# Optimization experiments

Hardware: AMD Instinct MI355X
Metric: run time of the kernel (lower is better)

The kernel has to match this reference:

```python
import jax, jax.numpy as jnp
import numpy as np

HIDDEN = 4096
N_HEADS = 32
N_KV_HEADS = 8
HEAD_DIM = HIDDEN // N_HEADS  # 128
GROUPS = N_HEADS // N_KV_HEADS  # 4
ROPE_BASE = 10000.0
BATCH, SEQ = 1, 2048


def _rope_cos_sin(position_ids, dim, base):
    # position_ids: [b, s] int -> cos/sin [b, s, dim]
    inv_freq = 1.0 / (base ** (jnp.arange(0, dim, 2, dtype=jnp.float32) / dim))  # [dim/2]
    freqs = position_ids.astype(jnp.float32)[..., None] * inv_freq  # [b, s, dim/2]
    emb = jnp.concatenate([freqs, freqs], axis=-1)  # [b, s, dim]
    return jnp.cos(emb), jnp.sin(emb)


def _rotate_half(x):
    x1, x2 = jnp.split(x, 2, axis=-1)
    return jnp.concatenate([-x2, x1], axis=-1)


def setup_inputs() -> dict:
    key = jax.random.key(0)
    ks = jax.random.split(key, 8)
    s = 0.02
    return {
        'hidden_states': jax.random.normal(ks[0], (BATCH, SEQ, HIDDEN), dtype=jnp.float32),
        'position_ids': jnp.broadcast_to(jnp.arange(SEQ, dtype=jnp.int64), (BATCH, SEQ)),
        'Wq': jax.random.normal(ks[1], (HIDDEN, N_HEADS * HEAD_DIM), dtype=jnp.float32) * s,
        'bq': jax.random.normal(ks[2], (N_HEADS * HEAD_DIM,), dtype=jnp.float32) * s,
        'Wk': jax.random.normal(ks[3], (HIDDEN, N_KV_HEADS * HEAD_DIM), dtype=jnp.float32) * s,
        'bk': jax.random.normal(ks[4], (N_KV_HEADS * HEAD_DIM,), dtype=jnp.float32) * s,
        'Wv': jax.random.normal(ks[5], (HIDDEN, N_KV_HEADS * HEAD_DIM), dtype=jnp.float32) * s,
        'bv': jax.random.normal(ks[6], (N_KV_HEADS * HEAD_DIM,), dtype=jnp.float32) * s,
        'Wo': jax.random.normal(ks[7], (HIDDEN, HIDDEN), dtype=jnp.float32) * s,
    }


def reference(hidden_states, position_ids, Wq, bq, Wk, bk, Wv, bv, Wo):
    b, s, _ = hidden_states.shape
    # QKV projections (bias=True for q/k/v per module)
    q = hidden_states @ Wq + bq  # [b, s, H*d]
    k = hidden_states @ Wk + bk  # [b, s, Hk*d]
    v = hidden_states @ Wv + bv  # [b, s, Hk*d]
    q = q.reshape(b, s, N_HEADS, HEAD_DIM)
    k = k.reshape(b, s, N_KV_HEADS, HEAD_DIM)
    v = v.reshape(b, s, N_KV_HEADS, HEAD_DIM)

    # RoPE gathered by position_ids
    cos, sin = _rope_cos_sin(position_ids, HEAD_DIM, ROPE_BASE)  # [b, s, d]
    cos = cos[:, :, None, :]
    sin = sin[:, :, None, :]
    q = q * cos + _rotate_half(q) * sin
    k = k * cos + _rotate_half(k) * sin

    # GQA causal attention: group query heads over shared kv heads
    qg = q.reshape(b, s, N_KV_HEADS, GROUPS, HEAD_DIM)
    scale = 1.0 / jnp.sqrt(jnp.asarray(HEAD_DIM, dtype=q.dtype))
    scores = jnp.einsum('bqhgd,bkhd->bhgqk', qg, k) * scale  # [b, Hk, g, s, s]
    causal = jnp.tril(jnp.ones((s, s), dtype=bool))
    scores = jnp.where(causal, scores, jnp.finfo(scores.dtype).min)
    probs = jax.nn.softmax(scores, axis=-1)
    out = jnp.einsum('bhgqk,bkhd->bqhgd', probs, v)  # [b, s, Hk, g, d]
    out = out.reshape(b, s, HIDDEN)
    return out @ Wo  # o_proj, bias=False
```

## Files before the change

kernel.cpp:

```cpp
#include <hip/hip_runtime.h>
#include <hip/hip_bf16.h>

typedef __hip_bfloat16 bf16;
typedef __attribute__((ext_vector_type(8))) __bf16 bf16x8;
typedef __attribute__((ext_vector_type(4))) float f32x4;

#define SEQ 2048
#define HID 4096
#define NH 32
#define NKV 8
#define HD 128
#define KVDIM 1024
#define QKVN 6144

#define MiB (1024 * 1024)

__device__ __forceinline__ void gl_lds16(const void* g, void* lds) {
  __builtin_amdgcn_global_load_lds((const __attribute__((address_space(1))) void*)g,
                                   (__attribute__((address_space(3))) void*)lds,
                                   16, 0, 0);
}

__device__ __forceinline__ float unplo(unsigned u) { return __uint_as_float(u << 16); }
__device__ __forceinline__ float unphi(unsigned u) { return __uint_as_float(u & 0xffff0000u); }
__device__ __forceinline__ unsigned packbf(float a, float b) {
  bf16 t[2] = {__float2bfloat16(a), __float2bfloat16(b)};
  return *reinterpret_cast<unsigned*>(t);
}

__global__ void cvt_kernel(const float* __restrict__ in, bf16* __restrict__ out, int n) {
  int i = (blockIdx.x * blockDim.x + threadIdx.x) * 4;
  if (i >= n) return;
  float4 v = *reinterpret_cast<const float4*>(in + i);
  bf16 o[4] = {__float2bfloat16(v.x), __float2bfloat16(v.y),
               __float2bfloat16(v.z), __float2bfloat16(v.w)};
  *reinterpret_cast<short4*>(out + i) = *reinterpret_cast<const short4*>(o);
}

__global__ void concat_bias_kernel(const float* __restrict__ bq, const float* __restrict__ bk,
                                   const float* __restrict__ bv, float* __restrict__ o) {
  int i = blockIdx.x * blockDim.x + threadIdx.x;
  if (i >= QKVN) return;
  o[i] = (i < HID) ? bq[i] : (i < HID + KVDIM ? bk[i - HID] : bv[i - HID - KVDIM]);
}

__global__ void transpose_qkvw_kernel(const float* __restrict__ Wq, const float* __restrict__ Wk,
                                      const float* __restrict__ Wv, bf16* __restrict__ Wqkvt) {
  __shared__ float tile[32][33];
  int t = blockIdx.x;
  const float* in;
  bf16* out;
  int si, xt, yt;
  if (t < 16384)      { in = Wq; out = Wqkvt;                           si = HID;   xt = t & 127; yt = t >> 7; }
  else if (t < 20480) { t -= 16384; in = Wk; out = Wqkvt + (size_t)HID * HID;           si = KVDIM; xt = t & 31; yt = t >> 5; }
  else                { t -= 20480; in = Wv; out = Wqkvt + (size_t)(HID + KVDIM) * HID; si = KVDIM; xt = t & 31; yt = t >> 5; }
  int c0 = xt * 32, r0 = yt * 32;
  int tx = threadIdx.x, ty = threadIdx.y;
#pragma unroll
  for (int i = 0; i < 32; i += 8)
    tile[ty + i][tx] = in[(size_t)(r0 + ty + i) * si + (c0 + tx)];
  __syncthreads();
#pragma unroll
  for (int i = 0; i < 32; i += 8)
    out[(size_t)(c0 + ty + i) * HID + (r0 + tx)] = __float2bfloat16(tile[tx][ty + i]);
}

__global__ void postqkv_kernel(const bf16* __restrict__ Ch, bf16* __restrict__ Qb,
                               bf16* __restrict__ Kb, bf16* __restrict__ Vt) {
  __shared__ float tile[32][33];
  int b = blockIdx.x;
  int tid = threadIdx.x;
  if (b < 10240) {
    bool isQ = (b < 8192);
    int idx = (isQ ? b : b - 8192) * 256 + tid;
    int j = idx & 31;
    int h = (idx >> 5) & (isQ ? 31 : 7);
    int s = idx >> (isQ ? 10 : 8);
    size_t bi = (size_t)s * QKVN + (isQ ? 0 : HID) + h * HD;
    unsigned u1 = *reinterpret_cast<const unsigned*>(Ch + bi + 2 * j);
    unsigned u2 = *reinterpret_cast<const unsigned*>(Ch + bi + 64 + 2 * j);
    float x1a = unplo(u1), x1b = unphi(u1);
    float x2a = unplo(u2), x2b = unphi(u2);
    float inv0 = __expf(-(float)(2 * j) * 0.14391156831212787f);
    float inv1 = __expf(-(float)(2 * j + 1) * 0.14391156831212787f);
    float sn0, cs0, sn1, cs1;
    __sincosf((float)s * inv0, &sn0, &cs0);
    __sincosf((float)s * inv1, &sn1, &cs1);
    size_t bo = (size_t)s * (isQ ? HID : KVDIM) + h * HD;
    bf16* Ob = isQ ? Qb : Kb;
    *reinterpret_cast<unsigned*>(Ob + bo + 2 * j) =
        packbf(x1a * cs0 - x2a * sn0, x1b * cs1 - x2b * sn1);
    *reinterpret_cast<unsigned*>(Ob + bo + 64 + 2 * j) =
        packbf(x2a * cs0 + x1a * sn0, x2b * cs1 + x1b * sn1);
  } else {
    int t = b - 10240;
    int xt = t & 31, yt = t >> 5;
    int tx = tid & 31, ty = tid >> 5;
#pragma unroll
    for (int i = 0; i < 32; i += 8)
      tile[ty + i][tx] = __bfloat162float(Ch[(size_t)(yt * 32 + ty + i) * QKVN + (HID + KVDIM) + xt * 32 + tx]);
    __syncthreads();
#pragma unroll
    for (int i = 0; i < 32; i += 8)
      Vt[(size_t)(xt * 32 + ty + i) * SEQ + (yt * 32 + tx)] = __float2bfloat16(tile[tx][ty + i]);
  }
}

#define BARRIER() __builtin_amdgcn_s_barrier()
#define LGKM0()                                          \
  {                                                      \
    asm volatile("s_waitcnt lgkmcnt(0)" ::: "memory");   \
    __builtin_amdgcn_sched_barrier(0);                   \
  }
#define MFMA_ACC(d, x, y) d = __builtin_amdgcn_mfma_f32_16x16x32_bf16(x, y, d, 0, 0, 0)

__global__ __launch_bounds__(512, 2) void gemm256_kernel(
    const bf16* __restrict__ A, const bf16* __restrict__ Bt,
    const float* __restrict__ bias, float* __restrict__ C0, float* __restrict__ C1,
    bf16* __restrict__ Ch, const float* __restrict__ WoSrc, bf16* __restrict__ WotDst,
    int N, int Ksub, int lda, int mode) {
  __shared__ bf16 lds[2][4][128 * 64];
  const int blk = blockIdx.x;
  int bx, by, bz;
  if (mode == 1) {
    if (blk >= 192) {
      float (*tile)[32][33] = reinterpret_cast<float(*)[32][33]>(&lds[0][0][0]);
      int k = blk - 192;
      int tid = threadIdx.x;
      int sub = tid >> 8, tx = tid & 31, ty = (tid >> 5) & 7;
      for (int p = 0; p < 128; ++p) {
        int t = k * 256 + p * 2 + sub;
        int xt = t & 127, yt = t >> 7;
#pragma unroll
        for (int i = 0; i < 32; i += 8)
          tile[sub][ty + i][tx] = WoSrc[(size_t)(yt * 32 + ty + i) * HID + xt * 32 + tx];
        __syncthreads();
#pragma unroll
        for (int i = 0; i < 32; i += 8)
          WotDst[(size_t)(xt * 32 + ty + i) * HID + (yt * 32 + tx)] =
              __float2bfloat16(tile[sub][tx][ty + i]);
        __syncthreads();
      }
      return;
    }
    bx = blk % 24; by = blk / 24; bz = 0;
  } else {
    bz = blk >> 7;
    int rem = blk & 127;
    bx = rem & 15; by = rem >> 4;
  }
  const int tid = threadIdx.x;
  const int lane = tid & 63;
  const int w = tid >> 6;
  const int wr = w >> 2, wc = w & 3;
  const int m0 = by * 256;
  const int n0 = bx * 256;
  const bf16* Ab = A + (size_t)bz * Ksub;
  const bf16* Btb = Bt + (size_t)bz * Ksub;
  const int nt = Ksub >> 6;

#define STAGE(buf, half, t)                                                     \
  {                                                                             \
    const bf16* _s = ((half) < 2) ? Ab : Btb;                                   \
    int _g0 = (((half) < 2) ? m0 : n0) + ((half) & 1) * 128;                    \
    _Pragma("unroll")                                                           \
    for (int _it = 0; _it < 2; ++_it) {                                         \
      int _row = w * 16 + _it * 8 + (lane >> 3);                                \
      int _ch = (lane & 7) ^ (_row & 7);                                        \
      gl_lds16(_s + (size_t)(_g0 + _row) * lda + (size_t)(t) * 64 + _ch * 8,    \
               &lds[buf][half][(w * 16 + _it * 8) * 64]);                       \
    }                                                                           \
  }

  auto rdA = [&](int cur, int mi, int ks) {
    int rr = mi * 16 + (lane & 15);
    int byt = rr * 128 + (((ks * 32 + (lane >> 4) * 8) * 2) ^ ((rr & 7) << 4));
    return *reinterpret_cast<const bf16x8*>(
        reinterpret_cast<const char*>(&lds[cur][wr][0]) + byt);
  };
  auto rdB = [&](int cur, int ni, int ks) {
    int rr = (wc & 1) * 64 + ni * 16 + (lane & 15);
    int byt = rr * 128 + (((ks * 32 + (lane >> 4) * 8) * 2) ^ ((rr & 7) << 4));
    return *reinterpret_cast<const bf16x8*>(
        reinterpret_cast<const char*>(&lds[cur][2 + (wc >> 1)][0]) + byt);
  };

  f32x4 acc[8][4];
  const f32x4 z = {0.f, 0.f, 0.f, 0.f};
#pragma unroll
  for (int i = 0; i < 8; ++i)
#pragma unroll
    for (int j = 0; j < 4; ++j) acc[i][j] = z;

  STAGE(0, 0, 0); STAGE(0, 1, 0); STAGE(0, 2, 0); STAGE(0, 3, 0);
  STAGE(1, 2, 1); STAGE(1, 3, 1); STAGE(1, 0, 1);
  asm volatile("s_waitcnt vmcnt(6)" ::: "memory");
  BARRIER();

  bf16x8 a[4][2], b[4][2];
  int cur = 0;
  for (int t = 0; t < nt; ++t, cur ^= 1) {
#pragma unroll
    for (int mi = 0; mi < 4; ++mi) { a[mi][0] = rdA(cur, mi, 0); a[mi][1] = rdA(cur, mi, 1); }
#pragma unroll
    for (int ni = 0; ni < 2; ++ni) { b[ni][0] = rdB(cur, ni, 0); b[ni][1] = rdB(cur, ni, 1); }
    if (t + 1 < nt) STAGE(cur ^ 1, 1, t + 1);
    BARRIER();
    LGKM0();
    __builtin_amdgcn_s_setprio(1);
#pragma unroll
    for (int mi = 0; mi < 4; ++mi)
#pragma unroll
      for (int ni = 0; ni < 2; ++ni) {
        MFMA_ACC(acc[mi][ni], a[mi][0], b[ni][0]);
        MFMA_ACC(acc[mi][ni], a[mi][1], b[ni][1]);
      }
    __builtin_amdgcn_s_setprio(0);
    BARRIER();
#pragma unroll
    for (int ni = 2; ni < 4; ++ni) { b[ni][0] = rdB(cur, ni, 0); b[ni][1] = rdB(cur, ni, 1); }
    BARRIER();
    LGKM0();
    __builtin_amdgcn_s_setprio(1);
#pragma unroll
    for (int mi = 0; mi < 4; ++mi)
#pragma unroll
      for (int ni = 2; ni < 4; ++ni) {
        MFMA_ACC(acc[mi][ni], a[mi][0], b[ni][0]);
        MFMA_ACC(acc[mi][ni], a[mi][1], b[ni][1]);
      }
    __builtin_amdgcn_s_setprio(0);
    BARRIER();
#pragma unroll
    for (int mi = 0; mi < 4; ++mi) { a[mi][0] = rdA(cur, mi + 4, 0); a[mi][1] = rdA(cur, mi + 4, 1); }
    if (t + 2 < nt) { STAGE(cur, 2, t + 2); STAGE(cur, 3, t + 2); }
    BARRIER();
    LGKM0();
    __builtin_amdgcn_s_setprio(1);
#pragma unroll
    for (int mi = 0; mi < 4; ++mi)
#pragma unroll
      for (int ni = 2; ni < 4; ++ni) {
        MFMA_ACC(acc[mi + 4][ni], a[mi][0], b[ni][0]);
        MFMA_ACC(acc[mi + 4][ni], a[mi][1], b[ni][1]);
      }
    __builtin_amdgcn_s_setprio(0);
    BARRIER();
    if (t + 2 < nt) STAGE(cur, 0, t + 2);
    if (t + 2 < nt) {
      asm volatile("s_waitcnt vmcnt(6)" ::: "memory");
    } else if (t + 1 < nt) {
      asm volatile("s_waitcnt vmcnt(0)" ::: "memory");
    }
    BARRIER();
    __builtin_amdgcn_s_setprio(1);
#pragma unroll
    for (int mi = 0; mi < 4; ++mi)
#pragma unroll
      for (int ni = 0; ni < 2; ++ni) {
        MFMA_ACC(acc[mi + 4][ni], a[mi][0], b[ni][0]);
        MFMA_ACC(acc[mi + 4][ni], a[mi][1], b[ni][1]);
      }
    __builtin_amdgcn_s_setprio(0);
    BARRIER();
  }

  if (mode == 1) {
#pragma unroll
    for (int ni = 0; ni < 4; ++ni) {
      int col = n0 + wc * 64 + ni * 16 + (lane & 15);
      float bv = bias[col];
#pragma unroll
      for (int mi = 0; mi < 8; ++mi) {
        int rbase = m0 + wr * 128 + mi * 16 + (lane >> 4) * 4;
#pragma unroll
        for (int r = 0; r < 4; ++r)
          Ch[(size_t)(rbase + r) * N + col] = __float2bfloat16(acc[mi][ni][r] + bv);
      }
    }
  } else {
    float* Cb = bz ? C1 : C0;
#pragma unroll
    for (int ni = 0; ni < 4; ++ni) {
      int col = n0 + wc * 64 + ni * 16 + (lane & 15);
#pragma unroll
      for (int mi = 0; mi < 8; ++mi) {
        int rbase = m0 + wr * 128 + mi * 16 + (lane >> 4) * 4;
#pragma unroll
        for (int r = 0; r < 4; ++r)
          Cb[(size_t)(rbase + r) * N + col] = acc[mi][ni][r];
      }
    }
  }
#undef STAGE
}

__global__ void reduce_kernel(const float* __restrict__ P0, const float* __restrict__ P1,
                              float* __restrict__ out, int n) {
  int i = (blockIdx.x * blockDim.x + threadIdx.x) * 4;
  if (i >= n) return;
  float4 a = *reinterpret_cast<const float4*>(P0 + i);
  float4 b = *reinterpret_cast<const float4*>(P1 + i);
  float4 o = {a.x + b.x, a.y + b.y, a.z + b.z, a.w + b.w};
  *reinterpret_cast<float4*>(out + i) = o;
}

__global__ __launch_bounds__(256) void attn_kernel(
    const bf16* __restrict__ Q,
    const bf16* __restrict__ Kb,
    const bf16* __restrict__ Vt,
    bf16* __restrict__ AO,
    float* __restrict__ Opart,
    float* __restrict__ Ml) {
  __shared__ bf16 Ks[64 * 128];
  __shared__ bf16 Vs[128 * 64];
  __shared__ bf16 Ps[4][16 * 64];
  const int tid = threadIdx.x, lane = tid & 63, w = tid >> 6;
  const int b = blockIdx.x;
  const int H = b & 31;
  const int tt = b >> 5;
  int qb, lo, hi, half;
  bool split;
  if (tt < 32) {
    qb = 16 + ((31 - tt) >> 1);
    half = tt & 1;
    int n = qb + 1, mid = n >> 1;
    lo = half ? mid : 0;
    hi = half ? n : mid;
    split = true;
  } else {
    qb = 47 - tt;
    half = 0;
    lo = 0;
    hi = qb + 1;
    split = false;
  }
  const int kvh = H >> 2;
  const int qw = qb * 64 + w * 16;
  const int hig = lane >> 4;
  const int q_loc = lane & 15;
  const int qa = qw + q_loc;

  bf16x8 aq[4];
#pragma unroll
  for (int kd = 0; kd < 4; ++kd) {
    int row = qw + q_loc;
    int d = kd * 32 + hig * 8;
    aq[kd] = *reinterpret_cast<const bf16x8*>(Q + (size_t)row * HID + H * HD + d);
  }

  float m_run = -1e30f, l_run = 0.0f;
  f32x4 o[8];
  const f32x4 z = {0.f, 0.f, 0.f, 0.f};
#pragma unroll
  for (int dt = 0; dt < 8; ++dt) o[dt] = z;

  const float scale = 0.08838834764831845f;

  for (int t = lo; t < hi; ++t) {
    int kvbase = t * 64;
#pragma unroll
    for (int it = 0; it < 4; ++it) {
      int c = w * 4 + it;
      int row = c * 4 + (lane >> 4);
      int sb = ((lane & 15) * 16) ^ ((row & 7) << 4);
      gl_lds16(Kb + (size_t)(kvbase + row) * KVDIM + kvh * HD + (sb >> 1), &Ks[c * 512]);
    }
#pragma unroll
    for (int it = 0; it < 4; ++it) {
      int c = w * 4 + it;
      int row = c * 8 + (lane >> 3);
      int sb = ((lane & 7) * 16) ^ ((row & 7) << 4);
      gl_lds16(Vt + (size_t)(kvh * HD + row) * SEQ + kvbase + (sb >> 1), &Vs[c * 512]);
    }
    __syncthreads();

    f32x4 sf[4];
#pragma unroll
    for (int j = 0; j < 4; ++j) sf[j] = z;
#pragma unroll
    for (int j = 0; j < 4; ++j) {
#pragma unroll
      for (int kd = 0; kd < 4; ++kd) {
        int r = j * 16 + q_loc;
        int byt = r * 256 + (((kd * 32 + hig * 8) * 2) ^ ((r & 7) << 4));
        bf16x8 kfr = *reinterpret_cast<const bf16x8*>(reinterpret_cast<const char*>(Ks) + byt);
        sf[j] = __builtin_amdgcn_mfma_f32_16x16x32_bf16(kfr, aq[kd], sf[j], 0, 0, 0);
      }
    }

    float vals[4][4];
    bool diag = (t == qb);
#pragma unroll
    for (int j = 0; j < 4; ++j)
#pragma unroll
      for (int r = 0; r < 4; ++r) {
        float v = sf[j][r] * scale;
        if (diag) {
          int ka = kvbase + j * 16 + hig * 4 + r;
          if (ka > qa) v = -1e30f;
        }
        vals[j][r] = v;
      }

    float m01 = fmaxf(fmaxf(vals[0][0], vals[0][1]), fmaxf(vals[0][2], vals[0][3]));
    float m23 = fmaxf(fmaxf(vals[1][0], vals[1][1]), fmaxf(vals[1][2], vals[1][3]));
    float m45 = fmaxf(fmaxf(vals[2][0], vals[2][1]), fmaxf(vals[2][2], vals[2][3]));
    float m67 = fmaxf(fmaxf(vals[3][0], vals[3][1]), fmaxf(vals[3][2], vals[3][3]));
    float m = fmaxf(fmaxf(m01, m23), fmaxf(m45, m67));
    m = fmaxf(m, __shfl_xor(m, 16));
    m = fmaxf(m, __shfl_xor(m, 32));
    float mn = fmaxf(m_run, m);
    float alpha = __expf(m_run - mn);
    m_run = mn;

    float p[4][4];
    float rs = 0.0f;
#pragma unroll
    for (int j = 0; j < 4; ++j)
#pragma unroll
      for (int r = 0; r < 4; ++r) {
        p[j][r] = __expf(vals[j][r] - mn);
        rs += p[j][r];
      }
    rs += __shfl_xor(rs, 16);
    rs += __shfl_xor(rs, 32);
    l_run = l_run * alpha + rs;

#pragma unroll
    for (int j = 0; j < 4; ++j) {
      bf16 tmp[4] = {__float2bfloat16(p[j][0]), __float2bfloat16(p[j][1]),
                     __float2bfloat16(p[j][2]), __float2bfloat16(p[j][3])};
      int coff = (j * 16 + hig * 4) * 2;
      int byt = q_loc * 128 + (coff ^ ((q_loc & 7) << 4));
      *reinterpret_cast<uint2*>(reinterpret_cast<char*>(&Ps[w][0]) + byt) =
          *reinterpret_cast<const uint2*>(tmp);
    }

#pragma unroll
    for (int r = 0; r < 4; ++r) {
      float alr = __shfl(alpha, hig * 4 + r);
#pragma unroll
      for (int dt = 0; dt < 8; ++dt) o[dt][r] *= alr;
    }

    bf16x8 pa[2];
#pragma unroll
    for (int ks = 0; ks < 2; ++ks) {
      int byt = q_loc * 128 + (((ks * 32 + hig * 8) * 2) ^ ((q_loc & 7) << 4));
      pa[ks] = *reinterpret_cast<const bf16x8*>(reinterpret_cast<const char*>(&Ps[w][0]) + byt);
    }
#pragma unroll
    for (int dt = 0; dt < 8; ++dt)
#pragma unroll
      for (int ks = 0; ks < 2; ++ks) {
        int vrow = dt * 16 + q_loc;
        int byt = vrow * 128 + (((ks * 32 + hig * 8) * 2) ^ ((vrow & 7) << 4));
        bf16x8 vb = *reinterpret_cast<const bf16x8*>(reinterpret_cast<const char*>(Vs) + byt);
        o[dt] = __builtin_amdgcn_mfma_f32_16x16x32_bf16(pa[ks], vb, o[dt], 0, 0, 0);
      }
    __syncthreads();
  }

  if (!split) {
#pragma unroll
    for (int r = 0; r < 4; ++r) {
      float li = __shfl(l_run, hig * 4 + r);
      float linv = 1.0f / li;
#pragma unroll
      for (int dt = 0; dt < 8; ++dt) {
        int qrow = qw + hig * 4 + r;
        int d = dt * 16 + q_loc;
        AO[(size_t)qrow * HID + H * HD + d] = __float2bfloat16(o[dt][r] * linv);
      }
    }
  } else {
    size_t pbase = ((size_t)(half * NH + H) * 1024);
#pragma unroll
    for (int dt = 0; dt < 8; ++dt)
#pragma unroll
      for (int r = 0; r < 4; ++r) {
        int qrow = qw + hig * 4 + r;
        int d = dt * 16 + q_loc;
        Opart[(pbase + (qrow - 1024)) * HD + d] = o[dt][r];
      }
    if (lane < 16) {
      Ml[(pbase + (qa - 1024)) * 2 + 0] = m_run;
      Ml[(pbase + (qa - 1024)) * 2 + 1] = l_run;
    }
  }
}

__global__ __launch_bounds__(256) void merge_kernel(
    const float* __restrict__ Opart, const float* __restrict__ Ml,
    bf16* __restrict__ AO) {
  int i = blockIdx.x * 256 + threadIdx.x;
  int dq = (i & 31) << 2;
  int row = (i >> 5) & 1023;
  int H = i >> 15;
  size_t b1 = (size_t)H * 1024 + row;
  size_t b2 = (size_t)(NH + H) * 1024 + row;
  float m1 = Ml[b1 * 2], l1 = Ml[b1 * 2 + 1];
  float m2 = Ml[b2 * 2], l2 = Ml[b2 * 2 + 1];
  float M = fmaxf(m1, m2);
  float w1 = __expf(m1 - M), w2 = __expf(m2 - M);
  float inv = 1.0f / (l1 * w1 + l2 * w2);
  float4 o1 = *reinterpret_cast<const float4*>(Opart + b1 * HD + dq);
  float4 o2 = *reinterpret_cast<const float4*>(Opart + b2 * HD + dq);
  bf16 o[4] = {__float2bfloat16((o1.x * w1 + o2.x * w2) * inv),
               __float2bfloat16((o1.y * w1 + o2.y * w2) * inv),
               __float2bfloat16((o1.z * w1 + o2.z * w2) * inv),
               __float2bfloat16((o1.w * w1 + o2.w * w2) * inv)};
  *reinterpret_cast<short4*>(AO + (size_t)(1024 + row) * HID + H * HD + dq) =
      *reinterpret_cast<const short4*>(o);
}

extern "C" void kernel_launch(void* const* d_in, const int* in_sizes, int n_in,
                              void* d_out, int out_size, void* d_ws, size_t ws_size,
                              hipStream_t stream) {
  const float* hidden = (const float*)d_in[0];
  const float* Wq = (const float*)d_in[2];
  const float* bq = (const float*)d_in[3];
  const float* Wk = (const float*)d_in[4];
  const float* bk = (const float*)d_in[5];
  const float* Wv = (const float*)d_in[6];
  const float* bv = (const float*)d_in[7];
  const float* Wo = (const float*)d_in[8];
  float* out = (float*)d_out;

  char* ws = (char*)d_ws;
  bf16*  Wqkvt  = (bf16*)(ws + (size_t)0 * MiB);
  bf16*  Xb     = (bf16*)(ws + (size_t)48 * MiB);
  bf16*  Cqkvh  = (bf16*)(ws + (size_t)64 * MiB);
  bf16*  Wot    = (bf16*)(ws + (size_t)88 * MiB);
  bf16*  Qb     = (bf16*)(ws + (size_t)120 * MiB);
  bf16*  Kb     = (bf16*)(ws + (size_t)136 * MiB);
  bf16*  Vt     = (bf16*)(ws + (size_t)140 * MiB);
  float* bqkv   = (float*)Qb;
  bf16*  AO     = Cqkvh;
  float* Opart  = (float*)Wqkvt;
  float* Ml     = (float*)(ws + (size_t)48 * MiB);
  float* P0     = (float*)Wqkvt;
  float* P1     = (float*)(ws + (size_t)16 * MiB);
  P1 = (float*)(ws + (size_t)32 * MiB);

  cvt_kernel<<<(SEQ * HID) / 1024, 256, 0, stream>>>(hidden, Xb, SEQ * HID);
  concat_bias_kernel<<<QKVN / 256, 256, 0, stream>>>(bq, bk, bv, bqkv);
  transpose_qkvw_kernel<<<24576, dim3(32, 8), 0, stream>>>(Wq, Wk, Wv, Wqkvt);

  gemm256_kernel<<<256, 512, 0, stream>>>(
      Xb, Wqkvt, bqkv, nullptr, nullptr, Cqkvh, Wo, Wot, QKVN, HID, HID, 1);

  postqkv_kernel<<<12288, 256, 0, stream>>>(Cqkvh, Qb, Kb, Vt);

  attn_kernel<<<1536, 256, 0, stream>>>(Qb, Kb, Vt, AO, Opart, Ml);
  merge_kernel<<<(NH * 1024 * 32) / 256, 256, 0, stream>>>(Opart, Ml, AO);

  gemm256_kernel<<<256, 512, 0, stream>>>(
      AO, Wot, nullptr, P0, P1, nullptr, nullptr, nullptr, HID, 2048, HID, 0);
  reduce_kernel<<<(SEQ * HID) / 1024, 256, 0, stream>>>(P0, P1, out, SEQ * HID);
}
```

Before: 358.0 us.

## Move Wo transpose into weight-transpose kernel and use a 128x128 GEMM for o_proj

Wo is now transposed to bf16 inside the shared weight-transpose kernel instead of by 64 extra blocks piggybacked on the QKV GEMM launch, so the QKV GEMM launches only its 192 compute blocks and drops its mode branching. The output projection switches from the 256x256 double-buffered GEMM (256 blocks, split-K 2) to a simpler single-buffered 128x128 tile kernel with 1024 blocks, still split-K 2. The aim is better load balance and CU fill for o_proj and removing the straggler transpose blocks from the QKV GEMM. The trade-off is that the new kernel has no LDS double buffering, so loads and MFMAs may not overlap as well.

```diff
diff --git a/kernel.cpp b/kernel.cpp
--- a/kernel.cpp
+++ b/kernel.cpp
@@ -44,8 +44,9 @@
   o[i] = (i < HID) ? bq[i] : (i < HID + KVDIM ? bk[i - HID] : bv[i - HID - KVDIM]);
 }
 
-__global__ void transpose_qkvw_kernel(const float* __restrict__ Wq, const float* __restrict__ Wk,
-                                      const float* __restrict__ Wv, bf16* __restrict__ Wqkvt) {
+__global__ void transpose_all_kernel(const float* __restrict__ Wq, const float* __restrict__ Wk,
+                                     const float* __restrict__ Wv, const float* __restrict__ Wo,
+                                     bf16* __restrict__ Wqkvt, bf16* __restrict__ Wot) {
   __shared__ float tile[32][33];
   int t = blockIdx.x;
   const float* in;
@@ -53,7 +54,8 @@
   int si, xt, yt;
   if (t < 16384)      { in = Wq; out = Wqkvt;                           si = HID;   xt = t & 127; yt = t >> 7; }
   else if (t < 20480) { t -= 16384; in = Wk; out = Wqkvt + (size_t)HID * HID;           si = KVDIM; xt = t & 31; yt = t >> 5; }
-  else                { t -= 20480; in = Wv; out = Wqkvt + (size_t)(HID + KVDIM) * HID; si = KVDIM; xt = t & 31; yt = t >> 5; }
+  else if (t < 24576) { t -= 20480; in = Wv; out = Wqkvt + (size_t)(HID + KVDIM) * HID; si = KVDIM; xt = t & 31; yt = t >> 5; }
+  else                { t -= 24576; in = Wo; out = Wot;                 si = HID;   xt = t & 127; yt = t >> 7; }
   int c0 = xt * 32, r0 = yt * 32;
   int tx = threadIdx.x, ty = threadIdx.y;
 #pragma unroll
@@ -116,47 +118,19 @@
 
 __global__ __launch_bounds__(512, 2) void gemm256_kernel(
     const bf16* __restrict__ A, const bf16* __restrict__ Bt,
-    const float* __restrict__ bias, float* __restrict__ C0, float* __restrict__ C1,
-    bf16* __restrict__ Ch, const float* __restrict__ WoSrc, bf16* __restrict__ WotDst,
-    int N, int Ksub, int lda, int mode) {
+    const float* __restrict__ bias, bf16* __restrict__ Ch,
+    int N, int Ksub, int lda) {
   __shared__ bf16 lds[2][4][128 * 64];
   const int blk = blockIdx.x;
-  int bx, by, bz;
-  if (mode == 1) {
-    if (blk >= 192) {
-      float (*tile)[32][33] = reinterpret_cast<float(*)[32][33]>(&lds[0][0][0]);
-      int k = blk - 192;
-      int tid = threadIdx.x;
-      int sub = tid >> 8, tx = tid & 31, ty = (tid >> 5) & 7;
-      for (int p = 0; p < 128; ++p) {
-        int t = k * 256 + p * 2 + sub;
-        int xt = t & 127, yt = t >> 7;
-#pragma unroll
-        for (int i = 0; i < 32; i += 8)
-          tile[sub][ty + i][tx] = WoSrc[(size_t)(yt * 32 + ty + i) * HID + xt * 32 + tx];
-        __syncthreads();
-#pragma unroll
-        for (int i = 0; i < 32; i += 8)
-          WotDst[(size_t)(xt * 32 + ty + i) * HID + (yt * 32 + tx)] =
-              __float2bfloat16(tile[sub][tx][ty + i]);
-        __syncthreads();
-      }
-      return;
-    }
-    bx = blk % 24; by = blk / 24; bz = 0;
-  } else {
-    bz = blk >> 7;
-    int rem = blk & 127;
-    bx = rem & 15; by = rem >> 4;
-  }
+  const int bx = blk % 24, by = blk / 24;
   const int tid = threadIdx.x;
   const int lane = tid & 63;
   const int w = tid >> 6;
   const int wr = w >> 2, wc = w & 3;
   const int m0 = by * 256;
   const int n0 = bx * 256;
-  const bf16* Ab = A + (size_t)bz * Ksub;
-  const bf16* Btb = Bt + (size_t)bz * Ksub;
+  const bf16* Ab = A;
+  const bf16* Btb = Bt;
   const int nt = Ksub >> 6;
 
 #define STAGE(buf, half, t)                                                     \
@@ -265,34 +239,89 @@
     BARRIER();
   }
 
-  if (mode == 1) {
-#pragma unroll
-    for (int ni = 0; ni < 4; ++ni) {
-      int col = n0 + wc * 64 + ni * 16 + (lane & 15);
-      float bv = bias[col];
-#pragma unroll
-      for (int mi = 0; mi < 8; ++mi) {
-        int rbase = m0 + wr * 128 + mi * 16 + (lane >> 4) * 4;
-#pragma unroll
-        for (int r = 0; r < 4; ++r)
-          Ch[(size_t)(rbase + r) * N + col] = __float2bfloat16(acc[mi][ni][r] + bv);
-      }
-    }
-  } else {
-    float* Cb = bz ? C1 : C0;
-#pragma unroll
-    for (int ni = 0; ni < 4; ++ni) {
-      int col = n0 + wc * 64 + ni * 16 + (lane & 15);
-#pragma unroll
-      for (int mi = 0; mi < 8; ++mi) {
-        int rbase = m0 + wr * 128 + mi * 16 + (lane >> 4) * 4;
-#pragma unroll
-        for (int r = 0; r < 4; ++r)
-          Cb[(size_t)(rbase + r) * N + col] = acc[mi][ni][r];
-      }
+#pragma unroll
+  for (int ni = 0; ni < 4; ++ni) {
+    int col = n0 + wc * 64 + ni * 16 + (lane & 15);
+    float bv = bias[col];
+#pragma unroll
+    for (int mi = 0; mi < 8; ++mi) {
+      int rbase = m0 + wr * 128 + mi * 16 + (lane >> 4) * 4;
+#pragma unroll
+      for (int r = 0; r < 4; ++r)
+        Ch[(size_t)(rbase + r) * N + col] = __float2bfloat16(acc[mi][ni][r] + bv);
     }
   }
 #undef STAGE
+}
+
+__global__ __launch_bounds__(256) void gemm_bt_kernel(
+    const bf16* __restrict__ A, const bf16* __restrict__ Bt,
+    float* __restrict__ C0, float* __restrict__ C1,
+    int N, int Ksub, int lda) {
+  __shared__ bf16 As[128 * 64];
+  __shared__ bf16 Bs[128 * 64];
+  const int tid = threadIdx.x;
+  const int lane = tid & 63;
+  const int w = tid >> 6;
+  const int wm = w >> 1, wn = w & 1;
+  const int m0 = blockIdx.y * 128;
+  const int n0 = blockIdx.x * 128;
+  const int bz = blockIdx.z;
+  const bf16* Ab = A + (size_t)bz * Ksub;
+  const bf16* Btb = Bt + (size_t)bz * Ksub;
+  float* Cb = bz ? C1 : C0;
+
+  f32x4 acc[4][4];
+  const f32x4 z = {0.f, 0.f, 0.f, 0.f};
+#pragma unroll
+  for (int i = 0; i < 4; i++)
+#pragma unroll
+    for (int j = 0; j < 4; j++) acc[i][j] = z;
+
+  for (int kk = 0; kk < Ksub; kk += 64) {
+#pragma unroll
+    for (int it = 0; it < 4; ++it) {
+      int c = w * 4 + it;
+      int row = c * 8 + (lane >> 3);
+      int sb = ((lane & 7) * 16) ^ ((row & 7) << 4);
+      gl_lds16(Ab + (size_t)(m0 + row) * lda + kk + (sb >> 1), &As[c * 512]);
+      gl_lds16(Btb + (size_t)(n0 + row) * lda + kk + (sb >> 1), &Bs[c * 512]);
+    }
+    __syncthreads();
+#pragma unroll
+    for (int ks = 0; ks < 64; ks += 32) {
+      bf16x8 a[4], b[4];
+#pragma unroll
+      for (int mi = 0; mi < 4; ++mi) {
+        int r = wm * 64 + mi * 16 + (lane & 15);
+        int byt = r * 128 + (((ks + (lane >> 4) * 8) * 2) ^ ((r & 7) << 4));
+        a[mi] = *reinterpret_cast<const bf16x8*>(reinterpret_cast<const char*>(As) + byt);
+      }
+#pragma unroll
+      for (int ni = 0; ni < 4; ++ni) {
+        int r = wn * 64 + ni * 16 + (lane & 15);
+        int byt = r * 128 + (((ks + (lane >> 4) * 8) * 2) ^ ((r & 7) << 4));
+        b[ni] = *reinterpret_cast<const bf16x8*>(reinterpret_cast<const char*>(Bs) + byt);
+      }
+#pragma unroll
+      for (int mi = 0; mi < 4; ++mi)
+#pragma unroll
+        for (int ni = 0; ni < 4; ++ni)
+          acc[mi][ni] = __builtin_amdgcn_mfma_f32_16x16x32_bf16(a[mi], b[ni], acc[mi][ni], 0, 0, 0);
+    }
+    __syncthreads();
+  }
+#pragma unroll
+  for (int ni = 0; ni < 4; ++ni) {
+    int col = n0 + wn * 64 + ni * 16 + (lane & 15);
+#pragma unroll
+    for (int mi = 0; mi < 4; ++mi) {
+      int rbase = m0 + wm * 64 + mi * 16 + (lane >> 4) * 4;
+#pragma unroll
+      for (int r = 0; r < 4; ++r)
+        Cb[(size_t)(rbase + r) * N + col] = acc[mi][ni][r];
+    }
+  }
 }
 
 __global__ void reduce_kernel(const float* __restrict__ P0, const float* __restrict__ P1,
@@ -541,22 +570,20 @@
   float* Opart  = (float*)Wqkvt;
   float* Ml     = (float*)(ws + (size_t)48 * MiB);
   float* P0     = (float*)Wqkvt;
-  float* P1     = (float*)(ws + (size_t)16 * MiB);
-  P1 = (float*)(ws + (size_t)32 * MiB);
+  float* P1     = (float*)(ws + (size_t)32 * MiB);
 
   cvt_kernel<<<(SEQ * HID) / 1024, 256, 0, stream>>>(hidden, Xb, SEQ * HID);
   concat_bias_kernel<<<QKVN / 256, 256, 0, stream>>>(bq, bk, bv, bqkv);
-  transpose_qkvw_kernel<<<24576, dim3(32, 8), 0, stream>>>(Wq, Wk, Wv, Wqkvt);
-
-  gemm256_kernel<<<256, 512, 0, stream>>>(
-      Xb, Wqkvt, bqkv, nullptr, nullptr, Cqkvh, Wo, Wot, QKVN, HID, HID, 1);
+  transpose_all_kernel<<<40960, dim3(32, 8), 0, stream>>>(Wq, Wk, Wv, Wo, Wqkvt, Wot);
+
+  gemm256_kernel<<<192, 512, 0, stream>>>(Xb, Wqkvt, bqkv, Cqkvh, QKVN, HID, HID);
 
   postqkv_kernel<<<12288, 256, 0, stream>>>(Cqkvh, Qb, Kb, Vt);
 
   attn_kernel<<<1536, 256, 0, stream>>>(Qb, Kb, Vt, AO, Opart, Ml);
   merge_kernel<<<(NH * 1024 * 32) / 256, 256, 0, stream>>>(Opart, Ml, AO);
 
-  gemm256_kernel<<<256, 512, 0, stream>>>(
-      AO, Wot, nullptr, P0, P1, nullptr, nullptr, nullptr, HID, 2048, HID, 0);
+  gemm_bt_kernel<<<dim3(HID / 128, SEQ / 128, 2), 256, 0, stream>>>(
+      AO, Wot, P0, P1, HID, 2048, HID);
   reduce_kernel<<<(SEQ * HID) / 1024, 256, 0, stream>>>(P0, P1, out, SEQ * HID);
 }
```

Measured after the change: 377.7 us. 5.5% more time.
